# Kernel tuning notes

Hardware: AMD Instinct MI355X
Metric: run time of the kernel (lower is better)

Reference implementation:

```python
import jax, jax.numpy as jnp
import numpy as np

EMBED, HEADS, LEVELS, POINTS = 256, 8, 3, 4
SPATIAL = np.array([[128, 128], [64, 64], [32, 32]], dtype=np.int64)  # (H, W) per level
B = 2
S = int((SPATIAL[:, 0] * SPATIAL[:, 1]).sum())  # 21504
Q = S  # encoder self-attention: queries == flattened multi-scale features


def grid_sample_bilinear(img, grid):
    """img: [N,C,H,W]; grid: [N,Q,P,2] (x,y) in [-1,1]; bilinear, zeros padding, align_corners=False.
    Returns [N,C,Q,P]."""
    N, C, H, W = img.shape
    _, Qn, Pn, _ = grid.shape
    x = (grid[..., 0] + 1.0) * (W * 0.5) - 0.5
    y = (grid[..., 1] + 1.0) * (H * 0.5) - 0.5
    x0 = jnp.floor(x)
    y0 = jnp.floor(y)
    wx1 = x - x0
    wy1 = y - y0
    x0i = x0.astype(jnp.int32)
    y0i = y0.astype(jnp.int32)
    imgf = img.reshape(N, C, H * W)

    def gather(ix, iy):
        valid = (ix >= 0) & (ix < W) & (iy >= 0) & (iy < H)
        ixc = jnp.clip(ix, 0, W - 1)
        iyc = jnp.clip(iy, 0, H - 1)
        flat = (iyc * W + ixc).reshape(N, -1)  # [N, Q*P]
        v = jax.vmap(lambda im, f: im[:, f])(imgf, flat)  # [N, C, Q*P]
        return jnp.where(valid.reshape(N, 1, -1), v, 0.0)

    w00 = ((1.0 - wx1) * (1.0 - wy1)).reshape(N, 1, -1)
    w01 = (wx1 * (1.0 - wy1)).reshape(N, 1, -1)
    w10 = ((1.0 - wx1) * wy1).reshape(N, 1, -1)
    w11 = (wx1 * wy1).reshape(N, 1, -1)
    out = (gather(x0i, y0i) * w00 + gather(x0i + 1, y0i) * w01
           + gather(x0i, y0i + 1) * w10 + gather(x0i + 1, y0i + 1) * w11)
    return out.reshape(N, C, Qn, Pn)


def msda_forward(hidden_states, encoder_hidden_states, reference_points, shapes_np,
                 sampling_offsets_w, sampling_offsets_b, attention_weights_w, attention_weights_b,
                 value_proj_w, value_proj_b, output_proj_w, output_proj_b):
    Bn, Qn, E = hidden_states.shape
    H, L, P = HEADS, LEVELS, POINTS
    D = E // H
    Sn = encoder_hidden_states.shape[1]
    value = (encoder_hidden_states @ value_proj_w.T + value_proj_b).reshape(Bn, Sn, H, D)
    off = (hidden_states @ sampling_offsets_w.T + sampling_offsets_b).reshape(Bn, Qn, H, L, P, 2)
    aw = hidden_states @ attention_weights_w.T + attention_weights_b
    aw = jax.nn.softmax(aw.reshape(Bn, Qn, H, L * P), axis=-1).reshape(Bn, Qn, H, L, P)
    # offset normalizer is (W, H) per level
    norm = jnp.asarray(np.stack([shapes_np[:, 1], shapes_np[:, 0]], axis=-1), dtype=hidden_states.dtype)
    loc = reference_points[:, :, None, :, None, :] + off / norm[None, None, None, :, None, :]
    grids = 2.0 * loc - 1.0  # [B,Q,H,L,P,2]
    out = jnp.zeros((Bn * H, D, Qn), value.dtype)
    start = 0
    for lvl in range(L):  # small static loop over levels (distinct spatial shapes)
        h, w = int(shapes_np[lvl, 0]), int(shapes_np[lvl, 1])
        val_l = value[:, start:start + h * w].transpose(0, 2, 3, 1).reshape(Bn * H, D, h, w)
        start += h * w
        g = grids[:, :, :, lvl].transpose(0, 2, 1, 3, 4).reshape(Bn * H, Qn, P, 2)
        sampled = grid_sample_bilinear(val_l, g)  # [B*H, D, Q, P]
        w_l = aw[:, :, :, lvl].transpose(0, 2, 1, 3).reshape(Bn * H, 1, Qn, P)
        out = out + (sampled * w_l).sum(-1)
    out = out.reshape(Bn, H * D, Qn).transpose(0, 2, 1)  # [B,Q,E]
    return out @ output_proj_w.T + output_proj_b


def setup_inputs():
    key = jax.random.key(0)
    ks = jax.random.split(key, 11)
    sc = 0.02
    E, H, L, P = EMBED, HEADS, LEVELS, POINTS
    return {
        "hidden_states": jax.random.normal(ks[0], (B, Q, E), jnp.float32),
        "encoder_hidden_states": jax.random.normal(ks[1], (B, S, E), jnp.float32),
        "reference_points": jax.random.uniform(ks[2], (B, Q, L, 2), jnp.float32),
        "spatial_shapes": jnp.asarray(SPATIAL),
        "sampling_offsets_w": jax.random.normal(ks[3], (H * L * P * 2, E), jnp.float32) * sc,
        "sampling_offsets_b": jax.random.normal(ks[4], (H * L * P * 2,), jnp.float32) * sc,
        "attention_weights_w": jax.random.normal(ks[5], (H * L * P, E), jnp.float32) * sc,
        "attention_weights_b": jax.random.normal(ks[6], (H * L * P,), jnp.float32) * sc,
        "value_proj_w": jax.random.normal(ks[7], (E, E), jnp.float32) * sc,
        "value_proj_b": jax.random.normal(ks[8], (E,), jnp.float32) * sc,
        "output_proj_w": jax.random.normal(ks[9], (E, E), jnp.float32) * sc,
        "output_proj_b": jax.random.normal(ks[10], (E,), jnp.float32) * sc,
    }


def reference(hidden_states, encoder_hidden_states, reference_points, spatial_shapes,
              sampling_offsets_w, sampling_offsets_b, attention_weights_w, attention_weights_b,
              value_proj_w, value_proj_b, output_proj_w, output_proj_b):
    shapes_np = np.asarray(spatial_shapes)  # static per-level (H, W)
    return msda_forward(hidden_states, encoder_hidden_states, reference_points, shapes_np,
                        sampling_offsets_w, sampling_offsets_b, attention_weights_w, attention_weights_b,
                        value_proj_w, value_proj_b, output_proj_w, output_proj_b)
```

## Files before the change

kernel.cpp:

```cpp
#include <hip/hip_runtime.h>
#include <hip/hip_bf16.h>

#define EMBED   256
#define HEADS   8
#define LEVELS  3
#define POINTS  4
#define BATCH   2
#define QLEN    21504
#define SLEN    21504
#define MTOT    (BATCH * QLEN)

typedef __attribute__((ext_vector_type(8))) short short8;
typedef __attribute__((ext_vector_type(4))) float f32x4;
typedef __attribute__((ext_vector_type(2))) float f32x2;

__device__ __forceinline__ short f2bf(float x) {
    unsigned u = __builtin_bit_cast(unsigned, x);
    u += 0x7fffu + ((u >> 16) & 1u);
    return (short)(u >> 16);
}
__device__ __forceinline__ f32x2 bfpair(unsigned u) {
    f32x2 r;
    r.x = __builtin_bit_cast(float, u << 16);
    r.y = __builtin_bit_cast(float, u & 0xffff0000u);
    return r;
}
__device__ __forceinline__ void async16(const void* g, void* l) {
    __builtin_amdgcn_global_load_lds((const __attribute__((address_space(1))) void*)g,
                                     (__attribute__((address_space(3))) void*)l, 16, 0, 0);
}

__global__ __launch_bounds__(256)
void pack_weights_kernel(const float* __restrict__ vW, const float* __restrict__ oW,
                         const float* __restrict__ soW, const float* __restrict__ awW,
                         const float* __restrict__ soB, const float* __restrict__ awB,
                         short* __restrict__ vWb, short* __restrict__ oWb,
                         short* __restrict__ soawWb, float* __restrict__ soawB)
{
    int i = blockIdx.x * 256 + threadIdx.x;
    if (i < 65536) {
        vWb[i] = f2bf(vW[i]);
    } else if (i < 131072) {
        int j = i - 65536;
        oWb[j] = f2bf(oW[j]);
    } else if (i < 204800) {
        int j = i - 131072;
        int row = j >> 8, k = j & 255;
        float v = (row < 192) ? soW[row * 256 + k] : awW[(row - 192) * 256 + k];
        soawWb[j] = f2bf(v);
    } else if (i < 205088) {
        int row = i - 204800;
        soawB[row] = (row < 192) ? soB[row] : awB[row - 192];
    }
}

__device__ __forceinline__
void astat_gemm(const short8* __restrict__ afr, const short* __restrict__ Wt,
                const float* __restrict__ bias, int ngroups, int gcols,
                int rowstrip, short* __restrict__ Ws,
                int mode, int ldc, void* __restrict__ Cout)
{
    const int tid  = threadIdx.x;
    const int lane = tid & 63;
    const int wv   = tid >> 6;
    const int m16  = lane & 15;
    const int ko   = lane >> 4;
    const int nch  = gcols * 32;
    const int r0   = rowstrip + wv * 16 + ko * 4;

    for (int gidx = 0; gidx < ngroups; ++gidx) {
        const int colbase = gidx * gcols;
        for (int c = tid; c < nch; c += 512) {
            const int colL = c >> 5;
            const int cw   = c & 31;
            const int csw  = (cw & 24) | ((cw ^ colL) & 7);
            async16(Wt + (((size_t)(colbase + colL)) << 8) + csw * 8, Ws + c * 8);
        }
        __syncthreads();
        const short8* Wvp = (const short8*)Ws;
        const int nct = gcols >> 4;
        for (int ct = 0; ct < nct; ++ct) {
            const int colL = ct * 16 + m16;
            f32x4 a = (f32x4)0.f;
            #pragma unroll
            for (int kt = 0; kt < 8; ++kt) {
                const int g = kt * 4 + ko;
                const int s = (g & 24) | ((g ^ colL) & 7);
                a = __builtin_amdgcn_mfma_f32_16x16x32_bf16(afr[kt], Wvp[colL * 32 + s], a, 0, 0, 0);
            }
            const int col = colbase + colL;
            const float bv = bias[col];
            if (mode == 1) {
                const int h = col >> 5, ch = col & 31;
                #pragma unroll
                for (int r = 0; r < 4; ++r) {
                    const int rg = r0 + r;
                    const int b  = (rg >= SLEN) ? 1 : 0;
                    const int sx = rg - b * SLEN;
                    ((short*)Cout)[(((size_t)(b * 8 + h)) * SLEN + sx) * 32 + ch] = f2bf(a[r] + bv);
                }
            } else {
                #pragma unroll
                for (int r = 0; r < 4; ++r)
                    ((float*)Cout)[(size_t)(r0 + r) * ldc + col] = a[r] + bv;
            }
        }
        __syncthreads();
    }
}

__global__ __launch_bounds__(512)
void proj_gemm_kernel(const float* __restrict__ enc, const short* __restrict__ vWb,
                      const float* __restrict__ vB, short* __restrict__ valb,
                      const float* __restrict__ hs, const short* __restrict__ soawWb,
                      const float* __restrict__ soawB, float* __restrict__ offaw)
{
    __shared__ short Ws[128 * 256];
    const int tid = threadIdx.x;
    const int lane = tid & 63, wv = tid >> 6;
    const int m16 = lane & 15, ko = lane >> 4;
    const int rowstrip = blockIdx.y * 128;
    const bool isVal = (blockIdx.x == 0);
    const float* A = isVal ? enc : hs;
    const int row = rowstrip + wv * 16 + m16;

    short8 afr[8];
    const float* Af = A + (size_t)row * 256 + ko * 8;
    #pragma unroll
    for (int kt = 0; kt < 8; ++kt) {
        float4 x = *(const float4*)(Af + kt * 32);
        float4 y = *(const float4*)(Af + kt * 32 + 4);
        short8 t;
        t[0] = f2bf(x.x); t[1] = f2bf(x.y); t[2] = f2bf(x.z); t[3] = f2bf(x.w);
        t[4] = f2bf(y.x); t[5] = f2bf(y.y); t[6] = f2bf(y.z); t[7] = f2bf(y.w);
        afr[kt] = t;
    }

    if (isVal) astat_gemm(afr, vWb,    vB,    2, 128, rowstrip, Ws, 1, 256, valb);
    else       astat_gemm(afr, soawWb, soawB, 3,  96, rowstrip, Ws, 0, 288, offaw);
}

__global__ __launch_bounds__(512)
void out_gemm_kernel(const short* __restrict__ A, const short* __restrict__ oWb,
                     const float* __restrict__ oB, float* __restrict__ C)
{
    __shared__ short Ws[128 * 256];
    const int tid = threadIdx.x;
    const int lane = tid & 63, wv = tid >> 6;
    const int m16 = lane & 15, ko = lane >> 4;
    const int rowstrip = blockIdx.x * 128;
    const int row = rowstrip + wv * 16 + m16;

    short8 afr[8];
    const short* Ab = A + (size_t)row * 256 + ko * 8;
    #pragma unroll
    for (int kt = 0; kt < 8; ++kt) afr[kt] = *(const short8*)(Ab + kt * 32);

    astat_gemm(afr, oWb, oB, 2, 128, rowstrip, Ws, 0, 256, C);
}

__global__ __launch_bounds__(256, 8)
void msda_sample_kernel(const short* __restrict__ value,
                        const float* __restrict__ offaw,
                        const float* __restrict__ ref,
                        short* __restrict__ attn)
{
    __shared__ int prep[32 * 76];

    const int tid = threadIdx.x;
    const int g   = tid >> 3;
    const int sub = tid & 7;
    const int t   = sub >> 2;

    const int blk = blockIdx.x;
    const int h   = blk & 7;
    const int j   = blk >> 3;
    const int b   = (j >= 672) ? 1 : 0;
    const int qc  = j - b * 672;
    const int q   = qc * 32 + g;
    const int bq  = b * QLEN + q;

    {
        const float* awp = offaw + (size_t)bq * 288 + 192 + h * 12;
        const float4 wa = *(const float4*)(awp);
        const float4 wb = *(const float4*)(awp + 4);
        const float4 wc = *(const float4*)(awp + 8);
        float w[12] = { wa.x, wa.y, wa.z, wa.w, wb.x, wb.y, wb.z, wb.w,
                        wc.x, wc.y, wc.z, wc.w };
        float mx = w[0];
        #pragma unroll
        for (int i = 1; i < 12; ++i) mx = fmaxf(mx, w[i]);
        float s = 0.f;
        #pragma unroll
        for (int i = 0; i < 12; ++i) s += __expf(w[i] - mx);
        const float inv = 1.f / s;

        const float* offp = offaw + (size_t)bq * 288 + h * 24;
        const float* refp = ref + (size_t)bq * 6;
        const int npts = (sub < 4) ? 2 : 1;
        #pragma unroll
        for (int it = 0; it < 2; ++it) {
            if (it >= npts) break;
            const int p  = sub + it * 8;
            const int l  = p >> 2;
            const int Wl = 128 >> l;
            const int st = (l == 0) ? 0 : (l == 1 ? 16384 : 20480);

            const float2 oxy = *(const float2*)(offp + p * 2);
            const float2 rxy = *(const float2*)(refp + 2 * l);
            const float ox = oxy.x, oy = oxy.y;
            const float rx = rxy.x, ry = rxy.y;
            const float a  = __expf(w[p] - mx) * inv;

            const float x = fmaf(rx, (float)Wl, ox - 0.5f);
            const float y = fmaf(ry, (float)Wl, oy - 0.5f);
            const float x0f = floorf(x), y0f = floorf(y);
            const int   x0  = (int)x0f,  y0  = (int)y0f;
            const float wx1 = x - x0f, wy1 = y - y0f;
            const float wx0 = 1.f - wx1, wy0 = 1.f - wy1;
            const bool vy0 = (unsigned)y0       < (unsigned)Wl;
            const bool vy1 = (unsigned)(y0 + 1) < (unsigned)Wl;

            const int xs = min(max(x0, 0), Wl - 2);
            const float wl0 = (xs == x0) ? wx0 : ((xs == x0 + 1) ? wx1 : 0.f);
            const float wl1 = (xs == x0) ? wx1 : ((xs + 1 == x0) ? wx0 : 0.f);

            const int hb = (b * 8 + h) * SLEN + st;
            const int o0 = vy0 ? (hb + y0 * Wl + xs) * 64       : 0;
            const int o1 = vy1 ? (hb + (y0 + 1) * Wl + xs) * 64 : 0;

            int* pp = &prep[g * 76 + p * 6];
            pp[0] = o0;
            pp[1] = o1;
            pp[2] = __builtin_bit_cast(int, vy0 ? wy0 * wl0 * a : 0.f);
            pp[3] = __builtin_bit_cast(int, vy0 ? wy0 * wl1 * a : 0.f);
            pp[4] = __builtin_bit_cast(int, vy1 ? wy1 * wl0 * a : 0.f);
            pp[5] = __builtin_bit_cast(int, vy1 ? wy1 * wl1 * a : 0.f);
        }
    }
    __syncthreads();

    const char* vbytes = (const char*)value;
    const unsigned subb = (unsigned)sub * 16u;
    f32x2 acc2[4];
    acc2[0] = (f32x2)0.f; acc2[1] = (f32x2)0.f;
    acc2[2] = (f32x2)0.f; acc2[3] = (f32x2)0.f;

    #pragma unroll
    for (int pb = 0; pb < 4; ++pb) {
        int4  v[6];
        float wgt[6];
        #pragma unroll
        for (int i = 0; i < 3; ++i) {
            const int p = pb * 3 + i;
            const int* pp = &prep[g * 76 + p * 6];
            const unsigned o0 = (unsigned)pp[0] + subb;
            const unsigned o1 = (unsigned)pp[1] + subb;
            wgt[2*i]   = __builtin_bit_cast(float, pp[2 + t]);
            wgt[2*i+1] = __builtin_bit_cast(float, pp[4 + t]);
            v[2*i]   = *(const int4*)(vbytes + (size_t)o0);
            v[2*i+1] = *(const int4*)(vbytes + (size_t)o1);
        }
        #pragma unroll
        for (int i = 0; i < 6; ++i) {
            f32x2 w2; w2.x = wgt[i]; w2.y = wgt[i];
            acc2[0] = __builtin_elementwise_fma(w2, bfpair((unsigned)v[i].x), acc2[0]);
            acc2[1] = __builtin_elementwise_fma(w2, bfpair((unsigned)v[i].y), acc2[1]);
            acc2[2] = __builtin_elementwise_fma(w2, bfpair((unsigned)v[i].z), acc2[2]);
            acc2[3] = __builtin_elementwise_fma(w2, bfpair((unsigned)v[i].w), acc2[3]);
        }
    }

    #pragma unroll
    for (int j2 = 0; j2 < 4; ++j2) {
        acc2[j2].x += __shfl_xor(acc2[j2].x, 4);
        acc2[j2].y += __shfl_xor(acc2[j2].y, 4);
    }

    if (sub < 4) {
        int4 o;
        o.x = ((unsigned)(unsigned short)f2bf(acc2[0].y) << 16) | (unsigned short)f2bf(acc2[0].x);
        o.y = ((unsigned)(unsigned short)f2bf(acc2[1].y) << 16) | (unsigned short)f2bf(acc2[1].x);
        o.z = ((unsigned)(unsigned short)f2bf(acc2[2].y) << 16) | (unsigned short)f2bf(acc2[2].x);
        o.w = ((unsigned)(unsigned short)f2bf(acc2[3].y) << 16) | (unsigned short)f2bf(acc2[3].x);
        ((int4*)attn)[(size_t)bq * 32 + h * 4 + sub] = o;
    }
}

extern "C" void kernel_launch(void* const* d_in, const int* in_sizes, int n_in,
                              void* d_out, int out_size, void* d_ws, size_t ws_size,
                              hipStream_t stream) {
    const float* hs  = (const float*)d_in[0];
    const float* enc = (const float*)d_in[1];
    const float* rp  = (const float*)d_in[2];
    const float* soW = (const float*)d_in[4];
    const float* soB = (const float*)d_in[5];
    const float* awW = (const float*)d_in[6];
    const float* awB = (const float*)d_in[7];
    const float* vW  = (const float*)d_in[8];
    const float* vB  = (const float*)d_in[9];
    const float* oW  = (const float*)d_in[10];
    const float* oB  = (const float*)d_in[11];
    float* out = (float*)d_out;

    const int M = MTOT;
    const size_t ME = (size_t)M * 256;

    short* valb   = (short*)d_ws;
    short* attnb  = valb + ME;
    float* offaw  = (float*)(attnb + ME);
    short* vWb    = (short*)(offaw + (size_t)M * 288);
    short* oWb    = vWb + 65536;
    short* soawWb = oWb + 65536;
    float* soawB  = (float*)(soawWb + 73728);

    pack_weights_kernel<<<dim3(802), dim3(256), 0, stream>>>(vW, oW, soW, awW, soB, awB,
                                                             vWb, oWb, soawWb, soawB);
    proj_gemm_kernel<<<dim3(2, M / 128), dim3(512), 0, stream>>>(enc, vWb, vB, valb,
                                                                 hs, soawWb, soawB, offaw);
    msda_sample_kernel<<<dim3(M / 4), dim3(256), 0, stream>>>(valb, offaw, rp, attnb);
    out_gemm_kernel<<<dim3(M / 128), dim3(512), 0, stream>>>(attnb, oWb, oB, out);
}
```

Baseline: 240.7 us.

## Give each wave two row tiles in projection GEMMs, shrink blocks to 64 rows

The projection and output GEMM kernels now use 128-thread blocks covering 64 rows, each wave holding two 16-row A fragments. Each B fragment loaded from LDS feeds two MFMAs, halving LDS traffic per MFMA. The weight tile staged in LDS shrinks to 64 columns (48 for offsets/weights), so more column groups and barriers are needed, and register pressure rises from the doubled A fragments and accumulators. The grid doubles in block count, and fewer threads cooperate on each async weight load.

```diff
diff --git a/kernel.cpp b/kernel.cpp
--- a/kernel.cpp
+++ b/kernel.cpp
@@ -55,10 +55,10 @@
 }
 
 __device__ __forceinline__
-void astat_gemm(const short8* __restrict__ afr, const short* __restrict__ Wt,
-                const float* __restrict__ bias, int ngroups, int gcols,
-                int rowstrip, short* __restrict__ Ws,
-                int mode, int ldc, void* __restrict__ Cout)
+void astat_gemm2(const short8 afr[2][8], const short* __restrict__ Wt,
+                 const float* __restrict__ bias, int ngroups, int gcols,
+                 int rowstrip, short* __restrict__ Ws,
+                 int mode, int ldc, void* __restrict__ Cout)
 {
     const int tid  = threadIdx.x;
     const int lane = tid & 63;
@@ -66,11 +66,11 @@
     const int m16  = lane & 15;
     const int ko   = lane >> 4;
     const int nch  = gcols * 32;
-    const int r0   = rowstrip + wv * 16 + ko * 4;
+    const int r0   = rowstrip + wv * 32 + ko * 4;
 
     for (int gidx = 0; gidx < ngroups; ++gidx) {
         const int colbase = gidx * gcols;
-        for (int c = tid; c < nch; c += 512) {
+        for (int c = tid; c < nch; c += 128) {
             const int colL = c >> 5;
             const int cw   = c & 31;
             const int csw  = (cw & 24) | ((cw ^ colL) & 7);
@@ -81,82 +81,99 @@
         const int nct = gcols >> 4;
         for (int ct = 0; ct < nct; ++ct) {
             const int colL = ct * 16 + m16;
-            f32x4 a = (f32x4)0.f;
+            f32x4 a0 = (f32x4)0.f;
+            f32x4 a1 = (f32x4)0.f;
             #pragma unroll
             for (int kt = 0; kt < 8; ++kt) {
                 const int g = kt * 4 + ko;
                 const int s = (g & 24) | ((g ^ colL) & 7);
-                a = __builtin_amdgcn_mfma_f32_16x16x32_bf16(afr[kt], Wvp[colL * 32 + s], a, 0, 0, 0);
+                const short8 bfrag = Wvp[colL * 32 + s];
+                a0 = __builtin_amdgcn_mfma_f32_16x16x32_bf16(afr[0][kt], bfrag, a0, 0, 0, 0);
+                a1 = __builtin_amdgcn_mfma_f32_16x16x32_bf16(afr[1][kt], bfrag, a1, 0, 0, 0);
             }
             const int col = colbase + colL;
             const float bv = bias[col];
             if (mode == 1) {
-                const int h = col >> 5, ch = col & 31;
+                const int hh = col >> 5, ch = col & 31;
                 #pragma unroll
-                for (int r = 0; r < 4; ++r) {
-                    const int rg = r0 + r;
-                    const int b  = (rg >= SLEN) ? 1 : 0;
-                    const int sx = rg - b * SLEN;
-                    ((short*)Cout)[(((size_t)(b * 8 + h)) * SLEN + sx) * 32 + ch] = f2bf(a[r] + bv);
+                for (int rt = 0; rt < 2; ++rt) {
+                    const f32x4 a = rt ? a1 : a0;
+                    #pragma unroll
+                    for (int r = 0; r < 4; ++r) {
+                        const int rg = r0 + rt * 16 + r;
+                        const int b  = (rg >= SLEN) ? 1 : 0;
+                        const int sx = rg - b * SLEN;
+                        ((short*)Cout)[(((size_t)(b * 8 + hh)) * SLEN + sx) * 32 + ch] = f2bf(a[r] + bv);
+                    }
                 }
             } else {
                 #pragma unroll
-                for (int r = 0; r < 4; ++r)
-                    ((float*)Cout)[(size_t)(r0 + r) * ldc + col] = a[r] + bv;
+                for (int rt = 0; rt < 2; ++rt) {
+                    const f32x4 a = rt ? a1 : a0;
+                    #pragma unroll
+                    for (int r = 0; r < 4; ++r)
+                        ((float*)Cout)[(size_t)(r0 + rt * 16 + r) * ldc + col] = a[r] + bv;
+                }
             }
         }
         __syncthreads();
     }
 }
 
-__global__ __launch_bounds__(512)
+__global__ __launch_bounds__(128, 2)
 void proj_gemm_kernel(const float* __restrict__ enc, const short* __restrict__ vWb,
                       const float* __restrict__ vB, short* __restrict__ valb,
                       const float* __restrict__ hs, const short* __restrict__ soawWb,
                       const float* __restrict__ soawB, float* __restrict__ offaw)
 {
-    __shared__ short Ws[128 * 256];
+    __shared__ short Ws[64 * 256];
     const int tid = threadIdx.x;
     const int lane = tid & 63, wv = tid >> 6;
     const int m16 = lane & 15, ko = lane >> 4;
-    const int rowstrip = blockIdx.y * 128;
+    const int rowstrip = blockIdx.y * 64;
     const bool isVal = (blockIdx.x == 0);
     const float* A = isVal ? enc : hs;
-    const int row = rowstrip + wv * 16 + m16;
-
-    short8 afr[8];
-    const float* Af = A + (size_t)row * 256 + ko * 8;
+
+    short8 afr[2][8];
     #pragma unroll
-    for (int kt = 0; kt < 8; ++kt) {
-        float4 x = *(const float4*)(Af + kt * 32);
-        float4 y = *(const float4*)(Af + kt * 32 + 4);
-        short8 t;
-        t[0] = f2bf(x.x); t[1] = f2bf(x.y); t[2] = f2bf(x.z); t[3] = f2bf(x.w);
-        t[4] = f2bf(y.x); t[5] = f2bf(y.y); t[6] = f2bf(y.z); t[7] = f2bf(y.w);
-        afr[kt] = t;
-    }
-
-    if (isVal) astat_gemm(afr, vWb,    vB,    2, 128, rowstrip, Ws, 1, 256, valb);
-    else       astat_gemm(afr, soawWb, soawB, 3,  96, rowstrip, Ws, 0, 288, offaw);
-}
-
-__global__ __launch_bounds__(512)
+    for (int rt = 0; rt < 2; ++rt) {
+        const int row = rowstrip + wv * 32 + rt * 16 + m16;
+        const float* Af = A + (size_t)row * 256 + ko * 8;
+        #pragma unroll
+        for (int kt = 0; kt < 8; ++kt) {
+            float4 x = *(const float4*)(Af + kt * 32);
+            float4 y = *(const float4*)(Af + kt * 32 + 4);
+            short8 t;
+            t[0] = f2bf(x.x); t[1] = f2bf(x.y); t[2] = f2bf(x.z); t[3] = f2bf(x.w);
+            t[4] = f2bf(y.x); t[5] = f2bf(y.y); t[6] = f2bf(y.z); t[7] = f2bf(y.w);
+            afr[rt][kt] = t;
+        }
+    }
+
+    if (isVal) astat_gemm2(afr, vWb,    vB,    4, 64, rowstrip, Ws, 1, 256, valb);
+    else       astat_gemm2(afr, soawWb, soawB, 6, 48, rowstrip, Ws, 0, 288, offaw);
+}
+
+__global__ __launch_bounds__(128, 2)
 void out_gemm_kernel(const short* __restrict__ A, const short* __restrict__ oWb,
                      const float* __restrict__ oB, float* __restrict__ C)
 {
-    __shared__ short Ws[128 * 256];
+    __shared__ short Ws[64 * 256];
     const int tid = threadIdx.x;
     const int lane = tid & 63, wv = tid >> 6;
     const int m16 = lane & 15, ko = lane >> 4;
-    const int rowstrip = blockIdx.x * 128;
-    const int row = rowstrip + wv * 16 + m16;
-
-    short8 afr[8];
-    const short* Ab = A + (size_t)row * 256 + ko * 8;
+    const int rowstrip = blockIdx.x * 64;
+
+    short8 afr[2][8];
     #pragma unroll
-    for (int kt = 0; kt < 8; ++kt) afr[kt] = *(const short8*)(Ab + kt * 32);
-
-    astat_gemm(afr, oWb, oB, 2, 128, rowstrip, Ws, 0, 256, C);
+    for (int rt = 0; rt < 2; ++rt) {
+        const int row = rowstrip + wv * 32 + rt * 16 + m16;
+        const short* Ab = A + (size_t)row * 256 + ko * 8;
+        #pragma unroll
+        for (int kt = 0; kt < 8; ++kt) afr[rt][kt] = *(const short8*)(Ab + kt * 32);
+    }
+
+    astat_gemm2(afr, oWb, oB, 4, 64, rowstrip, Ws, 0, 256, C);
 }
 
 __global__ __launch_bounds__(256, 8)
@@ -316,8 +333,8 @@
 
     pack_weights_kernel<<<dim3(802), dim3(256), 0, stream>>>(vW, oW, soW, awW, soB, awB,
                                                              vWb, oWb, soawWb, soawB);
-    proj_gemm_kernel<<<dim3(2, M / 128), dim3(512), 0, stream>>>(enc, vWb, vB, valb,
-                                                                 hs, soawWb, soawB, offaw);
+    proj_gemm_kernel<<<dim3(2, M / 64), dim3(128), 0, stream>>>(enc, vWb, vB, valb,
+                                                                hs, soawWb, soawB, offaw);
     msda_sample_kernel<<<dim3(M / 4), dim3(256), 0, stream>>>(valb, offaw, rp, attnb);
-    out_gemm_kernel<<<dim3(M / 128), dim3(512), 0, stream>>>(attnb, oWb, oB, out);
-}
+    out_gemm_kernel<<<dim3(M / 64), dim3(128), 0, stream>>>(attnb, oWb, oB, out);
+}
```

Measured after the change: 243.1 us. About the same (+1.0%).
